# Kernel optimization log

Hardware: AMD Instinct MI355X
Metric: run time of the kernel (lower is better)

The kernel has to match this reference:

```python
import jax, jax.numpy as jnp
import numpy as np

B, Q, D, H, EF = 64, 300, 512, 8, 4
DH = D // H            # 64, per-head dim for scores
DV = (D * EF) // H     # 256, per-head value dim


def setup_inputs() -> dict:
    key = jax.random.key(0)
    ks = jax.random.split(key, 10)
    s = 0.02
    return {
        "query_feats": jax.random.normal(ks[0], (B, Q, D), jnp.float32),
        "bias": jax.random.normal(ks[1], (1, H, Q, Q), jnp.float32),
        "W_gen": jax.random.normal(ks[2], (D, D), jnp.float32) * s,
        "b_gen": jax.random.normal(ks[3], (D,), jnp.float32) * s,
        "W_val": jax.random.normal(ks[4], (D, D * EF), jnp.float32) * s,
        "b_val": jax.random.normal(ks[5], (D * EF,), jnp.float32) * s,
        "W_out": jax.random.normal(ks[6], (D * EF, D), jnp.float32) * s,
        "b_out": jax.random.normal(ks[7], (D,), jnp.float32) * s,
        "weight_bank": jnp.ones((1, H, Q, Q), jnp.float32) / np.sqrt(DH).astype(np.float32),
    }


def reference(query_feats, bias, W_gen, b_gen, W_val, b_val, W_out, b_out, weight_bank):
    bs, nq, d = query_feats.shape
    h = weight_bank.shape[1]
    # params_generator -> dynamic mixing matrix M: [bs, h, dh, nq]
    M = (query_feats @ W_gen + b_gen).reshape(bs, nq, h, -1).transpose(0, 2, 3, 1)
    # value: [bs, h, nq, dv]
    value = (query_feats @ W_val + b_val).reshape(bs, nq, h, -1).transpose(0, 2, 1, 3)
    # queries split per head: [bs, h, nq, dh]
    q = query_feats.reshape(bs, nq, h, -1).transpose(0, 2, 1, 3)
    # scores: [bs, h, nq, nq], scaled by learned weight bank + bias, GELU (exact), softmax
    scores = jnp.einsum('bhqd,bhdk->bhqk', q, M) * weight_bank + bias
    attn = jax.nn.softmax(jax.nn.gelu(scores, approximate=False), axis=-1)
    out = jnp.einsum('bhqk,bhkv->bhqv', attn, value)
    out = out.transpose(0, 2, 1, 3).reshape(bs, nq, -1)
    out = out @ W_out + b_out
    return out + query_feats
```

## Files before the change

### kernel.cpp

```cpp
#include <hip/hip_runtime.h>
#include <hip/hip_bf16.h>

typedef __attribute__((ext_vector_type(4))) float f32x4;
typedef __attribute__((ext_vector_type(8))) short s16x8;
typedef __attribute__((ext_vector_type(4))) short s16x4;

#define MFMA16(A, B, C) __builtin_amdgcn_mfma_f32_16x16x32_bf16((A), (B), (C), 0, 0, 0)

#define GLDS16(gsrc, ldst) __builtin_amdgcn_global_load_lds(                   \
    (const __attribute__((address_space(1))) void*)(gsrc),                    \
    (__attribute__((address_space(3))) void*)(ldst), 16, 0, 0)

__device__ __forceinline__ ushort f2bf(float f) {
    __hip_bfloat16 h = __float2bfloat16(f);
    return *reinterpret_cast<ushort*>(&h);
}

__device__ __forceinline__ float gelu_exact(float x) {
    float z = 0.70710678118f * x;
    float az = fabsf(z);
    float t = 1.0f / fmaf(0.3275911f, az, 1.0f);
    float poly = t * (0.254829592f + t * (-0.284496736f + t * (1.421413741f +
                 t * (-1.453152027f + t * 1.061405429f))));
    float e = __expf(-az * az);
    float erfv = copysignf(1.0f - poly * e, z);
    return 0.5f * x * (1.0f + erfv);
}

__global__ void k_cvt(const float* __restrict__ in, ushort* __restrict__ out, int n) {
    int i = (blockIdx.x * 256 + threadIdx.x) * 4;
    if (i + 3 >= n) return;
    float4 v = *(const float4*)(in + i);
    ushort4 o;
    o.x = f2bf(v.x); o.y = f2bf(v.y); o.z = f2bf(v.z); o.w = f2bf(v.w);
    *(ushort4*)(out + i) = o;
}

__global__ void k_twT(const float* __restrict__ w, ushort* __restrict__ wt, int K, int N) {
    __shared__ float tile[32][33];
    int k0 = blockIdx.x * 32, n0 = blockIdx.y * 32;
    int tx = threadIdx.x & 31, ty = threadIdx.x >> 5;
    #pragma unroll
    for (int i = ty; i < 32; i += 8)
        tile[i][tx] = w[(size_t)(k0 + i) * N + n0 + tx];
    __syncthreads();
    #pragma unroll
    for (int i = ty; i < 32; i += 8)
        wt[(size_t)(n0 + i) * K + k0 + tx] = f2bf(tile[tx][i]);
}

__global__ void k_zeroV9(ushort* __restrict__ Vt) {
    int i = (blockIdx.x * 256 + threadIdx.x) * 8;
    int bh = i >> 13, within = i & 8191;
    s16x8 z = {0, 0, 0, 0, 0, 0, 0, 0};
    *(s16x8*)(Vt + ((size_t)bh * 10 + 9) * 8192 + within) = z;
}

template <int OUT>
__global__ __launch_bounds__(512, 2) void k_gemm256(const ushort* __restrict__ A,
                                                    const ushort* __restrict__ BT,
                                                    const float* __restrict__ b1,
                                                    const float* __restrict__ b2,
                                                    void* __restrict__ o1,
                                                    void* __restrict__ o2,
                                                    int K, int GY) {
    __shared__ __align__(16) ushort As[2][256 * 64];
    __shared__ __align__(16) ushort Bs[2][256 * 64];
    int id = blockIdx.x;
    int xcd = id & 7, s = id >> 3;
    int mxl = s / GY, ny = s - mxl * GY;
    int mx = xcd * 10 + mxl;
    if (mx >= 75) return;
    int m0 = mx * 256, n0g = ny * 256;

    int t = threadIdx.x, l = t & 63, w = t >> 6;
    int wr = w >> 2, wc = w & 3;
    int lr = l & 15, lg = l >> 4;

    int rsrc[4], ksrc[4];
    #pragma unroll
    for (int c8 = 0; c8 < 4; ++c8) {
        int o = (c8 * 512 + t) * 16;
        int op = o ^ (((o >> 7) & 7) << 4);
        rsrc[c8] = op >> 7;
        ksrc[c8] = (op & 127) >> 1;
    }

    auto stage = [&](int kt, int buf) {
        int k0 = kt * 64;
        ushort* AsB = &As[buf][0];
        ushort* BsB = &Bs[buf][0];
        #pragma unroll
        for (int c8 = 0; c8 < 4; ++c8) {
            int dst = (c8 * 512 + w * 64) * 8;
            GLDS16(A  + (size_t)(m0 + rsrc[c8]) * K + k0 + ksrc[c8], AsB + dst);
            GLDS16(BT + (size_t)(n0g + rsrc[c8]) * K + k0 + ksrc[c8], BsB + dst);
        }
    };

    f32x4 acc[8][4];
    #pragma unroll
    for (int i = 0; i < 8; ++i)
        #pragma unroll
        for (int j = 0; j < 4; ++j)
            acc[i][j] = (f32x4){0.f, 0.f, 0.f, 0.f};

    int NT = K >> 6;
    stage(0, 0);
    stage(1, 1);

    for (int kt = 0; kt < NT; ++kt) {
        if (kt + 1 < NT) asm volatile("s_waitcnt vmcnt(8)" ::: "memory");
        else             asm volatile("s_waitcnt vmcnt(0)" ::: "memory");
        __builtin_amdgcn_s_barrier();

        int cur = kt & 1;
        const char* Ab = (const char*)&As[cur][0];
        const char* Bb = (const char*)&Bs[cur][0];
        #pragma unroll
        for (int ks = 0; ks < 2; ++ks) {
            int kb = (ks * 64 + lg * 16) ^ ((lr & 7) << 4);
            s16x8 af[8], bfv[4];
            #pragma unroll
            for (int rt = 0; rt < 8; ++rt)
                af[rt] = *(const s16x8*)(Ab + (wr * 128 + rt * 16 + lr) * 128 + kb);
            #pragma unroll
            for (int ct = 0; ct < 4; ++ct)
                bfv[ct] = *(const s16x8*)(Bb + (wc * 64 + ct * 16 + lr) * 128 + kb);
            #pragma unroll
            for (int rt = 0; rt < 8; ++rt)
                #pragma unroll
                for (int ct = 0; ct < 4; ++ct)
                    acc[rt][ct] = MFMA16(af[rt], bfv[ct], acc[rt][ct]);
        }

        __builtin_amdgcn_s_barrier();
        if (kt + 2 < NT) stage(kt + 2, cur);
    }

    if (OUT == 0) {
        if (n0g < 512) {
            ushort* G = (ushort*)o1;
            #pragma unroll
            for (int rt = 0; rt < 8; ++rt)
                #pragma unroll
                for (int ct = 0; ct < 4; ++ct) {
                    int col = n0g + wc * 64 + ct * 16 + lr;
                    float bv = b1[col];
                    #pragma unroll
                    for (int rr = 0; rr < 4; ++rr) {
                        int row = m0 + wr * 128 + rt * 16 + lg * 4 + rr;
                        G[(size_t)row * 512 + col] = f2bf(acc[rt][ct][rr] + bv);
                    }
                }
        } else {
            ushort* Vt = (ushort*)o2;
            #pragma unroll
            for (int rt = 0; rt < 8; ++rt) {
                int rl0 = m0 + wr * 128 + rt * 16 + lg * 4;
                int bb = rl0 / 300, key0 = rl0 - bb * 300;
                #pragma unroll
                for (int ct = 0; ct < 4; ++ct) {
                    int colv = n0g - 512 + wc * 64 + ct * 16 + lr;
                    float bv = b2[colv];
                    int hh = colv >> 8, v = colv & 255;
                    s16x4 pw;
                    #pragma unroll
                    for (int rr = 0; rr < 4; ++rr)
                        pw[rr] = (short)f2bf(acc[rt][ct][rr] + bv);
                    size_t addr = (((size_t)(bb * 8 + hh) * 10 + (key0 >> 5)) * 8192)
                                  + v * 32 + (key0 & 31);
                    *(s16x4*)(Vt + addr) = pw;
                }
            }
        }
    } else {
        float* out = (float*)o1;
        #pragma unroll
        for (int rt = 0; rt < 8; ++rt)
            #pragma unroll
            for (int ct = 0; ct < 4; ++ct) {
                int col = n0g + wc * 64 + ct * 16 + lr;
                float bv = b1[col];
                #pragma unroll
                for (int rr = 0; rr < 4; ++rr) {
                    int row = m0 + wr * 128 + rt * 16 + lg * 4 + rr;
                    size_t idx = (size_t)row * 512 + col;
                    out[idx] = acc[rt][ct][rr] + bv + b2[idx];
                }
            }
    }
}

__global__ __launch_bounds__(256, 4) void k_attn(const ushort* __restrict__ qf_bf,
                                                 const ushort* __restrict__ G_bf,
                                                 const ushort* __restrict__ Vt,
                                                 const float* __restrict__ wb,
                                                 const float* __restrict__ bias,
                                                 ushort* __restrict__ O) {
    __shared__ __align__(16) ushort P[64 * 320];
    __shared__ float invL[64];
    int id = blockIdx.x;
    int xcd = id & 7, s = id >> 3;
    int h = s / 40; int r2 = s - h * 40;
    int bi = r2 / 5, qt = r2 - bi * 5;
    int b = xcd * 8 + bi;

    int t = threadIdx.x, l = t & 63, w = t >> 6;
    int lr = l & 15, lg = l >> 4;

    auto p_addr = [&](int q, int k) -> ushort* {
        int byte = (q * 640 + k * 2) ^ ((q & 15) << 4);
        return (ushort*)((char*)P + byte);
    };

    int qr = min(qt * 64 + w * 16 + lr, 299);
    const ushort* qp = qf_bf + ((size_t)(b * 300 + qr)) * 512 + h * 64 + lg * 8;
    s16x8 q0 = *(const s16x8*)(qp);
    s16x8 q1 = *(const s16x8*)(qp + 32);

    int qq = w * 16 + lr;
    float ssum = 0.f;
    #pragma unroll
    for (int kt = 0; kt < 19; ++kt) {
        int key = kt * 16 + lr;
        int kcl = min(key, 299);
        const ushort* gp = G_bf + ((size_t)(b * 300 + kcl)) * 512 + h * 64 + lg * 8;
        s16x8 g0 = *(const s16x8*)(gp);
        s16x8 g1 = *(const s16x8*)(gp + 32);
        f32x4 a = (f32x4){0.f, 0.f, 0.f, 0.f};
        a = MFMA16(g0, q0, a);
        a = MFMA16(g1, q1, a);
        int k0 = kt * 16 + lg * 4;
        int k0c = min(k0, 296);
        size_t bidx = ((size_t)h * 300 + qr) * 300 + k0c;
        float4 wv = *(const float4*)(wb + bidx);
        float4 bv = *(const float4*)(bias + bidx);
        bool vmask = (kt < 18) || (lg < 3);
        s16x4 pw;
        #pragma unroll
        for (int r = 0; r < 4; ++r) {
            float x = a[r] * (&wv.x)[r] + (&bv.x)[r];
            float p = vmask ? __expf(gelu_exact(x)) : 0.f;
            ssum += p;
            pw[r] = (short)f2bf(p);
        }
        *(s16x4*)p_addr(qq, k0) = pw;
    }
    *(s16x4*)p_addr(w * 16 + (l >> 2), 304 + (l & 3) * 4) = (s16x4){0, 0, 0, 0};

    ssum += __shfl_xor(ssum, 16);
    ssum += __shfl_xor(ssum, 32);
    if (lg == 0) invL[qq] = 1.0f / ssum;

    __syncthreads();

    f32x4 acc[4][4];
    #pragma unroll
    for (int qg = 0; qg < 4; ++qg)
        #pragma unroll
        for (int nt = 0; nt < 4; ++nt)
            acc[qg][nt] = (f32x4){0.f, 0.f, 0.f, 0.f};

    const ushort* vbase = Vt + (size_t)(b * 8 + h) * 81920
                          + (size_t)(w * 64) * 32 + lg * 8;
    #pragma unroll
    for (int kc = 0; kc < 10; ++kc) {
        s16x8 vb[4], pa[4];
        #pragma unroll
        for (int nt = 0; nt < 4; ++nt)
            vb[nt] = *(const s16x8*)(vbase + (size_t)kc * 8192 + (nt * 16 + lr) * 32);
        #pragma unroll
        for (int qg = 0; qg < 4; ++qg)
            pa[qg] = *(const s16x8*)p_addr(qg * 16 + lr, kc * 32 + lg * 8);
        #pragma unroll
        for (int qg = 0; qg < 4; ++qg)
            #pragma unroll
            for (int nt = 0; nt < 4; ++nt)
                acc[qg][nt] = MFMA16(pa[qg], vb[nt], acc[qg][nt]);
    }

    #pragma unroll
    for (int qg = 0; qg < 4; ++qg)
        #pragma unroll
        for (int r = 0; r < 4; ++r) {
            int qloc = qg * 16 + lg * 4 + r;
            int q = qt * 64 + qloc;
            if (q < 300) {
                float iv = invL[qloc];
                #pragma unroll
                for (int nt = 0; nt < 4; ++nt) {
                    int v = w * 64 + nt * 16 + lr;
                    O[((size_t)(b * 300 + q)) * 2048 + h * 256 + v] =
                        f2bf(acc[qg][nt][r] * iv);
                }
            }
        }
}

extern "C" void kernel_launch(void* const* d_in, const int* in_sizes, int n_in,
                              void* d_out, int out_size, void* d_ws, size_t ws_size,
                              hipStream_t stream) {
    const float* qf    = (const float*)d_in[0];
    const float* bias  = (const float*)d_in[1];
    const float* W_gen = (const float*)d_in[2];
    const float* b_gen = (const float*)d_in[3];
    const float* W_val = (const float*)d_in[4];
    const float* b_val = (const float*)d_in[5];
    const float* W_out = (const float*)d_in[6];
    const float* b_out = (const float*)d_in[7];
    const float* wb    = (const float*)d_in[8];
    float* out = (float*)d_out;

    char* ws = (char*)d_ws;
    ushort* qf_bf = (ushort*)(ws);
    ushort* G_bf  = (ushort*)(ws + 19660800);
    ushort* Vt    = (ushort*)(ws + 39321600);
    ushort* O_bf  = (ushort*)(ws + 123207680);
    ushort* WgvT  = (ushort*)(ws + 201850880);
    ushort* WoT   = (ushort*)(ws + 204472320);

    k_cvt<<<dim3(9600), dim3(256), 0, stream>>>(qf, qf_bf, 9830400);
    k_twT<<<dim3(16, 16), dim3(256), 0, stream>>>(W_gen, WgvT, 512, 512);
    k_twT<<<dim3(16, 64), dim3(256), 0, stream>>>(W_val, WgvT + 512 * 512, 512, 2048);
    k_twT<<<dim3(64, 16), dim3(256), 0, stream>>>(W_out, WoT, 2048, 512);
    k_zeroV9<<<dim3(2048), dim3(256), 0, stream>>>(Vt);

    k_gemm256<0><<<dim3(800), dim3(512), 0, stream>>>(qf_bf, WgvT, b_gen, b_val,
                                                      G_bf, Vt, 512, 10);

    k_attn<<<dim3(2560), dim3(256), 0, stream>>>(qf_bf, G_bf, Vt, wb, bias, O_bf);

    k_gemm256<2><<<dim3(160), dim3(512), 0, stream>>>(O_bf, WoT, b_out, qf,
                                                      out, nullptr, 2048, 2);
}
```

Before: 309.7 us.

## Merge prep kernels into one launch and split attention PV loop into halves

Folds the bf16 conversion, three weight transposes and the V padding zeroing into a single k_prep launch dispatched by block index, removing four kernel launches and their gaps. In the attention kernel, the P·V accumulation is split into two sequential halves over the value columns, halving the live accumulator registers so the kernel can hold more waves per CU. The cost is that the P tile in LDS is read twice, and the loop adds a little extra work.

Result: slower. 386.4 us (+24.8%).

```diff
diff --git a/kernel.cpp b/kernel.cpp
--- a/kernel.cpp
+++ b/kernel.cpp
@@ -27,18 +27,40 @@
     return 0.5f * x * (1.0f + erfv);
 }
 
-__global__ void k_cvt(const float* __restrict__ in, ushort* __restrict__ out, int n) {
-    int i = (blockIdx.x * 256 + threadIdx.x) * 4;
-    if (i + 3 >= n) return;
-    float4 v = *(const float4*)(in + i);
-    ushort4 o;
-    o.x = f2bf(v.x); o.y = f2bf(v.y); o.z = f2bf(v.z); o.w = f2bf(v.w);
-    *(ushort4*)(out + i) = o;
-}
-
-__global__ void k_twT(const float* __restrict__ w, ushort* __restrict__ wt, int K, int N) {
+__global__ __launch_bounds__(256) void k_prep(const float* __restrict__ qf,
+                                              ushort* __restrict__ qf_bf,
+                                              const float* __restrict__ W_gen,
+                                              const float* __restrict__ W_val,
+                                              const float* __restrict__ W_out,
+                                              ushort* __restrict__ WgvT,
+                                              ushort* __restrict__ WoT,
+                                              ushort* __restrict__ Vt) {
     __shared__ float tile[32][33];
-    int k0 = blockIdx.x * 32, n0 = blockIdx.y * 32;
+    int blk = blockIdx.x;
+    if (blk < 9600) {
+        int i = (blk * 256 + threadIdx.x) * 4;
+        float4 v = *(const float4*)(qf + i);
+        ushort4 o;
+        o.x = f2bf(v.x); o.y = f2bf(v.y); o.z = f2bf(v.z); o.w = f2bf(v.w);
+        *(ushort4*)(qf_bf + i) = o;
+        return;
+    }
+    blk -= 9600;
+    if (blk >= 2304) {
+        int i = ((blk - 2304) * 256 + threadIdx.x) * 8;
+        int bh = i >> 13, within = i & 8191;
+        s16x8 z = {0, 0, 0, 0, 0, 0, 0, 0};
+        *(s16x8*)(Vt + ((size_t)bh * 10 + 9) * 8192 + within) = z;
+        return;
+    }
+    const float* w; ushort* wt; int K, N, kx, ny;
+    if (blk < 256)       { w = W_gen; wt = WgvT;             K = 512;  N = 512;
+                           kx = blk & 15;          ny = blk >> 4; }
+    else if (blk < 1280) { w = W_val; wt = WgvT + 512 * 512; K = 512;  N = 2048;
+                           int b2 = blk - 256;  kx = b2 & 15; ny = b2 >> 4; }
+    else                 { w = W_out; wt = WoT;              K = 2048; N = 512;
+                           int b2 = blk - 1280; kx = b2 & 63; ny = b2 >> 6; }
+    int k0 = kx * 32, n0 = ny * 32;
     int tx = threadIdx.x & 31, ty = threadIdx.x >> 5;
     #pragma unroll
     for (int i = ty; i < 32; i += 8)
@@ -47,13 +69,6 @@
     #pragma unroll
     for (int i = ty; i < 32; i += 8)
         wt[(size_t)(n0 + i) * K + k0 + tx] = f2bf(tile[tx][i]);
-}
-
-__global__ void k_zeroV9(ushort* __restrict__ Vt) {
-    int i = (blockIdx.x * 256 + threadIdx.x) * 8;
-    int bh = i >> 13, within = i & 8191;
-    s16x8 z = {0, 0, 0, 0, 0, 0, 0, 0};
-    *(s16x8*)(Vt + ((size_t)bh * 10 + 9) * 8192 + within) = z;
 }
 
 template <int OUT>
@@ -255,47 +270,50 @@
 
     __syncthreads();
 
-    f32x4 acc[4][4];
-    #pragma unroll
-    for (int qg = 0; qg < 4; ++qg)
-        #pragma unroll
-        for (int nt = 0; nt < 4; ++nt)
-            acc[qg][nt] = (f32x4){0.f, 0.f, 0.f, 0.f};
-
-    const ushort* vbase = Vt + (size_t)(b * 8 + h) * 81920
-                          + (size_t)(w * 64) * 32 + lg * 8;
-    #pragma unroll
-    for (int kc = 0; kc < 10; ++kc) {
-        s16x8 vb[4], pa[4];
-        #pragma unroll
-        for (int nt = 0; nt < 4; ++nt)
-            vb[nt] = *(const s16x8*)(vbase + (size_t)kc * 8192 + (nt * 16 + lr) * 32);
+    #pragma unroll 1
+    for (int half = 0; half < 2; ++half) {
+        f32x4 acc[4][2];
         #pragma unroll
         for (int qg = 0; qg < 4; ++qg)
-            pa[qg] = *(const s16x8*)p_addr(qg * 16 + lr, kc * 32 + lg * 8);
+            #pragma unroll
+            for (int nt = 0; nt < 2; ++nt)
+                acc[qg][nt] = (f32x4){0.f, 0.f, 0.f, 0.f};
+
+        const ushort* vb0 = Vt + (size_t)(b * 8 + h) * 81920
+                            + (size_t)(w * 64 + half * 32) * 32 + lg * 8;
+        #pragma unroll
+        for (int kc = 0; kc < 10; ++kc) {
+            s16x8 vb[2], pa[4];
+            #pragma unroll
+            for (int nt = 0; nt < 2; ++nt)
+                vb[nt] = *(const s16x8*)(vb0 + (size_t)kc * 8192 + (nt * 16 + lr) * 32);
+            #pragma unroll
+            for (int qg = 0; qg < 4; ++qg)
+                pa[qg] = *(const s16x8*)p_addr(qg * 16 + lr, kc * 32 + lg * 8);
+            #pragma unroll
+            for (int qg = 0; qg < 4; ++qg)
+                #pragma unroll
+                for (int nt = 0; nt < 2; ++nt)
+                    acc[qg][nt] = MFMA16(pa[qg], vb[nt], acc[qg][nt]);
+        }
+
         #pragma unroll
         for (int qg = 0; qg < 4; ++qg)
             #pragma unroll
-            for (int nt = 0; nt < 4; ++nt)
-                acc[qg][nt] = MFMA16(pa[qg], vb[nt], acc[qg][nt]);
-    }
-
-    #pragma unroll
-    for (int qg = 0; qg < 4; ++qg)
-        #pragma unroll
-        for (int r = 0; r < 4; ++r) {
-            int qloc = qg * 16 + lg * 4 + r;
-            int q = qt * 64 + qloc;
-            if (q < 300) {
-                float iv = invL[qloc];
-                #pragma unroll
-                for (int nt = 0; nt < 4; ++nt) {
-                    int v = w * 64 + nt * 16 + lr;
-                    O[((size_t)(b * 300 + q)) * 2048 + h * 256 + v] =
-                        f2bf(acc[qg][nt][r] * iv);
+            for (int r = 0; r < 4; ++r) {
+                int qloc = qg * 16 + lg * 4 + r;
+                int q = qt * 64 + qloc;
+                if (q < 300) {
+                    float iv = invL[qloc];
+                    #pragma unroll
+                    for (int nt = 0; nt < 2; ++nt) {
+                        int v = w * 64 + half * 32 + nt * 16 + lr;
+                        O[((size_t)(b * 300 + q)) * 2048 + h * 256 + v] =
+                            f2bf(acc[qg][nt][r] * iv);
+                    }
                 }
             }
-        }
+    }
 }
 
 extern "C" void kernel_launch(void* const* d_in, const int* in_sizes, int n_in,
@@ -320,11 +338,8 @@
     ushort* WgvT  = (ushort*)(ws + 201850880);
     ushort* WoT   = (ushort*)(ws + 204472320);
 
-    k_cvt<<<dim3(9600), dim3(256), 0, stream>>>(qf, qf_bf, 9830400);
-    k_twT<<<dim3(16, 16), dim3(256), 0, stream>>>(W_gen, WgvT, 512, 512);
-    k_twT<<<dim3(16, 64), dim3(256), 0, stream>>>(W_val, WgvT + 512 * 512, 512, 2048);
-    k_twT<<<dim3(64, 16), dim3(256), 0, stream>>>(W_out, WoT, 2048, 512);
-    k_zeroV9<<<dim3(2048), dim3(256), 0, stream>>>(Vt);
+    k_prep<<<dim3(13952), dim3(256), 0, stream>>>(qf, qf_bf, W_gen, W_val, W_out,
+                                                  WgvT, WoT, Vt);
 
     k_gemm256<0><<<dim3(800), dim3(512), 0, stream>>>(qf_bf, WgvT, b_gen, b_val,
                                                       G_bf, Vt, 512, 10);
```
